# Performance work log

Hardware: AMD Instinct MI355X
Metric: run time of the kernel (lower is better)

## Reference

```python
import jax, jax.numpy as jnp
import numpy as np

N = 10000
IN_DIM = 1024
HID = 128
LAT = 64
E = 320000


def setup_inputs() -> dict:
    key = jax.random.key(0)
    ks = jax.random.split(key, 12)
    def glorot(k, shape):
        lim = float(np.sqrt(6.0 / (shape[0] + shape[1])))
        return jax.random.uniform(k, shape, jnp.float32, -lim, lim)
    x = jax.random.normal(ks[0], (N, IN_DIM), jnp.float32)
    edge_index = jax.random.randint(ks[1], (2, E), 0, N, jnp.int64)
    return {
        "x": x,
        "edge_index": edge_index,
        "W_enc1": glorot(ks[2], (IN_DIM, HID)), "b_enc1": jnp.zeros((HID,), jnp.float32),
        "W_enc2": glorot(ks[3], (HID, LAT)),   "b_enc2": jnp.zeros((LAT,), jnp.float32),
        "W_att1": glorot(ks[4], (LAT, HID)),   "b_att1": jnp.zeros((HID,), jnp.float32),
        "W_att2": glorot(ks[5], (HID, IN_DIM)),"b_att2": jnp.zeros((IN_DIM,), jnp.float32),
        "W_str":  glorot(ks[6], (LAT, LAT)),   "b_str":  jnp.zeros((LAT,), jnp.float32),
    }


def _gcn_norm(edge_index, n):
    # PyG GCNConv default: add self-loops, symmetric normalization
    loop = jnp.arange(n, dtype=edge_index.dtype)
    send = jnp.concatenate([edge_index[0], loop])
    recv = jnp.concatenate([edge_index[1], loop])
    deg = jax.ops.segment_sum(jnp.ones_like(recv, dtype=jnp.float32), recv, num_segments=n)
    dis = jnp.where(deg > 0, jax.lax.rsqrt(deg), 0.0)
    norm = dis[send] * dis[recv]  # [E+N]
    return send, recv, norm


def _gcn(x, W, b, send, recv, norm, n):
    h = x @ W                                  # [N, out]
    msg = h[send] * norm[:, None]              # gather + scale
    agg = jax.ops.segment_sum(msg, recv, num_segments=n)  # scatter-add
    return agg + b


def reference(x, edge_index, W_enc1, b_enc1, W_enc2, b_enc2,
              W_att1, b_att1, W_att2, b_att2, W_str, b_str):
    n = x.shape[0]
    send, recv, norm = _gcn_norm(edge_index, n)
    # encoder
    h = jax.nn.relu(_gcn(x, W_enc1, b_enc1, send, recv, norm, n))
    z = jax.nn.relu(_gcn(h, W_enc2, b_enc2, send, recv, norm, n))
    # attribute decoder
    a = jax.nn.relu(_gcn(z, W_att1, b_att1, send, recv, norm, n))
    attr_recon = jax.nn.relu(_gcn(a, W_att2, b_att2, send, recv, norm, n))
    # structure decoder
    s = jax.nn.relu(_gcn(z, W_str, b_str, send, recv, norm, n))
    struct_recon = s @ s.T  # [N, N]
    return (attr_recon, struct_recon, z)
```

## Files before the change

### kernel.cpp

```cpp
#include <hip/hip_runtime.h>
#include <hip/hip_bf16.h>

#define IN_DIM 1024
#define HID 128
#define LAT 64
#define DEGPAD 128

typedef __attribute__((ext_vector_type(8))) short bf16x8;
typedef __attribute__((ext_vector_type(4))) short bf16x4;
typedef __attribute__((ext_vector_type(4))) float f32x4;

#define W1T_OFF 0
#define W2T_OFF 131072
#define Wa1T_OFF 139264
#define Wa2T_OFF 147456
#define WsT_OFF 278528
#define WT_TOTAL 282624

__device__ __forceinline__ void splitf(float v, __hip_bfloat16& h, __hip_bfloat16& l) {
    h = __float2bfloat16(v);
    l = __float2bfloat16(v - __bfloat162float(h));
}


template<int AMODE, bool BIAS, bool RELU, bool DIS, bool SPLITOUT, bool NT>
__device__ void dev_gemm(float* smem, int bx, int byy,
        const __hip_bfloat16* __restrict__ Ahi, const __hip_bfloat16* __restrict__ Alo,
        const float* __restrict__ Af,
        const __hip_bfloat16* __restrict__ Bthi, const __hip_bfloat16* __restrict__ Btlo,
        const float* __restrict__ bias, const int* __restrict__ cursor,
        float* __restrict__ Cf, __hip_bfloat16* __restrict__ Chi, __hip_bfloat16* __restrict__ Clo,
        int M, int K, int ldc) {
    int tid = threadIdx.x;
    int w = tid >> 6, lane = tid & 63;
    int wr = w >> 1, wc = w & 1;
    int m0 = byy * 128, n0 = bx * 64;
    int lrow = lane & 15, lk = (lane >> 4) * 8;

    int arow[4];
    size_t aoff[4];
#pragma unroll
    for (int mi = 0; mi < 4; ++mi) {
        arow[mi] = m0 + wr * 64 + mi * 16 + lrow;
        aoff[mi] = (size_t)arow[mi] * K + lk;
    }
    size_t boff[2];
#pragma unroll
    for (int nj = 0; nj < 2; ++nj)
        boff[nj] = (size_t)(n0 + wc * 32 + nj * 16 + lrow) * K + lk;

    f32x4 acc[4][2] = {};

    for (int k0 = 0; k0 < K; k0 += 32) {
        bf16x8 bh[2], bl[2], ah[4], al[4];
#pragma unroll
        for (int nj = 0; nj < 2; ++nj) {
            bh[nj] = *(const bf16x8*)(Bthi + boff[nj] + k0);
            bl[nj] = *(const bf16x8*)(Btlo + boff[nj] + k0);
        }
        if constexpr (AMODE == 0) {
#pragma unroll
            for (int mi = 0; mi < 4; ++mi) {
                ah[mi] = *(const bf16x8*)(Ahi + aoff[mi] + k0);
                al[mi] = *(const bf16x8*)(Alo + aoff[mi] + k0);
            }
        } else {
#pragma unroll
            for (int mi = 0; mi < 4; ++mi) {
                float4 f0 = make_float4(0.f, 0.f, 0.f, 0.f), f1 = f0;
                if (arow[mi] < M) {
                    f0 = *(const float4*)(Af + aoff[mi] + k0);
                    f1 = *(const float4*)(Af + aoff[mi] + k0 + 4);
                }
                float ff[8] = {f0.x, f0.y, f0.z, f0.w, f1.x, f1.y, f1.z, f1.w};
                __attribute__((aligned(16))) __hip_bfloat16 hb[8], lb[8];
#pragma unroll
                for (int t = 0; t < 8; ++t) splitf(ff[t], hb[t], lb[t]);
                ah[mi] = *(const bf16x8*)hb;
                al[mi] = *(const bf16x8*)lb;
            }
        }
#pragma unroll
        for (int mi = 0; mi < 4; ++mi)
#pragma unroll
            for (int nj = 0; nj < 2; ++nj) {
                acc[mi][nj] = __builtin_amdgcn_mfma_f32_16x16x32_bf16(ah[mi], bh[nj], acc[mi][nj], 0, 0, 0);
                acc[mi][nj] = __builtin_amdgcn_mfma_f32_16x16x32_bf16(ah[mi], bl[nj], acc[mi][nj], 0, 0, 0);
                acc[mi][nj] = __builtin_amdgcn_mfma_f32_16x16x32_bf16(al[mi], bh[nj], acc[mi][nj], 0, 0, 0);
            }
    }

    int r0 = (lane >> 4) * 4;
#pragma unroll
    for (int mi = 0; mi < 4; ++mi)
#pragma unroll
        for (int nj = 0; nj < 2; ++nj) {
            int cl = wc * 32 + nj * 16 + lrow;
#pragma unroll
            for (int r = 0; r < 4; ++r) {
                int rl = wr * 64 + mi * 16 + r0 + r;
                smem[rl * 68 + cl] = acc[mi][nj][r];
            }
        }
    __syncthreads();

#pragma unroll
    for (int it = 0; it < 8; ++it) {
        int rl = it * 16 + (tid >> 4);
        int c4 = tid & 15;
        int row = m0 + rl;
        if (row < M) {
            int col = n0 + c4 * 4;
            float4 v = *(const float4*)&smem[rl * 68 + c4 * 4];
            if (BIAS) {
                float4 b = *(const float4*)&bias[col];
                v.x += b.x; v.y += b.y; v.z += b.z; v.w += b.w;
            }
            if (RELU) {
                v.x = fmaxf(v.x, 0.f); v.y = fmaxf(v.y, 0.f);
                v.z = fmaxf(v.z, 0.f); v.w = fmaxf(v.w, 0.f);
            }
            if (DIS) {
                float di = rsqrtf((float)(cursor[row] + 1));
                v.x *= di; v.y *= di; v.z *= di; v.w *= di;
            }
            if constexpr (SPLITOUT) {
                float vv[4] = {v.x, v.y, v.z, v.w};
                __attribute__((aligned(8))) __hip_bfloat16 hs[4], ls[4];
#pragma unroll
                for (int k = 0; k < 4; ++k) splitf(vv[k], hs[k], ls[k]);
                *(bf16x4*)&Chi[(size_t)row * ldc + col] = *(bf16x4*)hs;
                *(bf16x4*)&Clo[(size_t)row * ldc + col] = *(bf16x4*)ls;
            } else if constexpr (NT) {
                __builtin_nontemporal_store(*(const f32x4*)&v, (f32x4*)&Cf[(size_t)row * ldc + col]);
            } else {
                *(float4*)&Cf[(size_t)row * ldc + col] = v;
            }
        }
    }
    __syncthreads();
}


__device__ void dev_sst(float* smem, int bi, int bj,
                        const __hip_bfloat16* __restrict__ Shi, const __hip_bfloat16* __restrict__ Slo,
                        float* __restrict__ C, int M) {
    int tid = threadIdx.x;
    int w = tid >> 6, lane = tid & 63;
    int wr = w >> 1, wc = w & 1;
    int i0 = bi * 128 + wr * 64;
    int j0 = bj * 128 + wc * 64;
    int lrow = lane & 15, lk = (lane >> 4) * 8;

    f32x4 acc[4][4] = {};
#pragma unroll
    for (int ks = 0; ks < 2; ++ks) {
        bf16x8 ah[4], al[4], bh[4], bl[4];
#pragma unroll
        for (int mi = 0; mi < 4; ++mi) {
            size_t off = (size_t)(i0 + mi * 16 + lrow) * 64 + ks * 32 + lk;
            ah[mi] = *(const bf16x8*)(Shi + off);
            al[mi] = *(const bf16x8*)(Slo + off);
        }
#pragma unroll
        for (int nj = 0; nj < 4; ++nj) {
            size_t off = (size_t)(j0 + nj * 16 + lrow) * 64 + ks * 32 + lk;
            bh[nj] = *(const bf16x8*)(Shi + off);
            bl[nj] = *(const bf16x8*)(Slo + off);
        }
#pragma unroll
        for (int mi = 0; mi < 4; ++mi)
#pragma unroll
            for (int nj = 0; nj < 4; ++nj) {
                acc[mi][nj] = __builtin_amdgcn_mfma_f32_16x16x32_bf16(ah[mi], bh[nj], acc[mi][nj], 0, 0, 0);
                acc[mi][nj] = __builtin_amdgcn_mfma_f32_16x16x32_bf16(ah[mi], bl[nj], acc[mi][nj], 0, 0, 0);
                acc[mi][nj] = __builtin_amdgcn_mfma_f32_16x16x32_bf16(al[mi], bh[nj], acc[mi][nj], 0, 0, 0);
            }
    }

    int r0 = (lane >> 4) * 4;

    if (bi != bj) {
#pragma unroll
        for (int mi = 0; mi < 4; ++mi)
#pragma unroll
            for (int nj = 0; nj < 4; ++nj) {
                int orow = j0 + nj * 16 + lrow;
                int ocol = i0 + mi * 16 + r0;
                if (orow < M && ocol < M) {
                    f32x4 v = acc[mi][nj];
                    __builtin_nontemporal_store(v, (f32x4*)&C[(size_t)orow * M + ocol]);
                }
            }
    }

#pragma unroll
    for (int p = 0; p < 2; ++p) {
        if (wc == p) {
#pragma unroll
            for (int mi = 0; mi < 4; ++mi)
#pragma unroll
                for (int nj = 0; nj < 4; ++nj) {
                    int cl = nj * 16 + lrow;
#pragma unroll
                    for (int r = 0; r < 4; ++r) {
                        int rl = wr * 64 + mi * 16 + r0 + r;
                        smem[rl * 68 + cl] = acc[mi][nj][r];
                    }
                }
        }
        __syncthreads();
#pragma unroll
        for (int it = 0; it < 8; ++it) {
            int rl = it * 16 + (tid >> 4);
            int c4 = tid & 15;
            int row = bi * 128 + rl;
            int col = bj * 128 + p * 64 + c4 * 4;
            if (row < M && col < M) {
                float4 v = *(const float4*)&smem[rl * 68 + c4 * 4];
                __builtin_nontemporal_store(*(const f32x4*)&v, (f32x4*)&C[(size_t)row * M + col]);
            }
        }
        __syncthreads();
    }
}


__global__ __launch_bounds__(256) void k_prep(const float* __restrict__ W1, const float* __restrict__ W2,
                                              const float* __restrict__ Wa1, const float* __restrict__ Wa2,
                                              const float* __restrict__ Ws,
                                              __hip_bfloat16* __restrict__ hi, __hip_bfloat16* __restrict__ lo,
                                              const int* __restrict__ ei, int* cursor,
                                              int* __restrict__ colPad, int E) {
    int gtid = blockIdx.x * 256 + threadIdx.x;
    int gsz = gridDim.x * 256;
    for (int e = gtid; e < E; e += gsz) {
        int s = ei[e], r = ei[E + e];
        int slot = atomicAdd(&cursor[r], 1);
        if (slot < DEGPAD) colPad[(size_t)r * DEGPAD + slot] = s;
    }
    for (int idx = gtid; idx < WT_TOTAL; idx += gsz) {
        const float* src; int base, shK, Nc;
        if (idx < W2T_OFF)       { src = W1;  base = W1T_OFF;  shK = 10; Nc = 128; }
        else if (idx < Wa1T_OFF) { src = W2;  base = W2T_OFF;  shK = 7;  Nc = 64; }
        else if (idx < Wa2T_OFF) { src = Wa1; base = Wa1T_OFF; shK = 6;  Nc = 128; }
        else if (idx < WsT_OFF)  { src = Wa2; base = Wa2T_OFF; shK = 7;  Nc = 1024; }
        else                     { src = Ws;  base = WsT_OFF;  shK = 6;  Nc = 64; }
        int local = idx - base;
        int nn = local >> shK;
        int k = local & ((1 << shK) - 1);
        splitf(src[(size_t)k * Nc + nn], hi[idx], lo[idx]);
    }
}

__global__ __launch_bounds__(256) void k_g1(const float* __restrict__ x,
                                            const __hip_bfloat16* __restrict__ Whi,
                                            const __hip_bfloat16* __restrict__ Wlo,
                                            const int* __restrict__ cursor,
                                            float* __restrict__ t128, int M) {
    __shared__ float smem[128 * 68];
    int t = blockIdx.x;
    dev_gemm<1, false, false, true, false, false>(smem, t & 1, t >> 1,
        nullptr, nullptr, x, Whi + W1T_OFF, Wlo + W1T_OFF, nullptr, cursor,
        t128, nullptr, nullptr, M, 1024, 128);
}

template<int F, bool BIAS, bool RELU, int OMODE>
__global__ __launch_bounds__(256) void k_spmm(const float* __restrict__ Hin,
                                              const int* __restrict__ colPad,
                                              const int* __restrict__ cursor,
                                              const float* __restrict__ bias,
                                              float* __restrict__ out, float* __restrict__ out2,
                                              __hip_bfloat16* __restrict__ ohi,
                                              __hip_bfloat16* __restrict__ olo, int n) {
    constexpr int JW = F / 64;
    int i = (blockIdx.x * 256 + threadIdx.x) >> 6;
    int lane = threadIdx.x & 63;
    if (i >= n) return;
    int d = cursor[i];
    float di = rsqrtf((float)(d + 1));
    if (d > DEGPAD) d = DEGPAD;
    const int* cp = colPad + (size_t)i * DEGPAD;
    float acc[JW];
    const float* self = Hin + (size_t)i * F;
#pragma unroll
    for (int j = 0; j < JW; ++j) acc[j] = self[lane + 64 * j];

    int p = 0;
    for (; p + 8 <= d; p += 8) {
        int4 ca = *(const int4*)(cp + p);
        int4 cb = *(const int4*)(cp + p + 4);
        int cc[8] = {ca.x, ca.y, ca.z, ca.w, cb.x, cb.y, cb.z, cb.w};
        float vals[8][JW];
#pragma unroll
        for (int q = 0; q < 8; ++q) {
            const float* row = Hin + (size_t)cc[q] * F;
#pragma unroll
            for (int j = 0; j < JW; ++j) vals[q][j] = row[lane + 64 * j];
        }
#pragma unroll
        for (int q = 0; q < 8; ++q)
#pragma unroll
            for (int j = 0; j < JW; ++j) acc[j] += vals[q][j];
    }
    for (; p + 4 <= d; p += 4) {
        int4 ca = *(const int4*)(cp + p);
        int cc[4] = {ca.x, ca.y, ca.z, ca.w};
        float vals[4][JW];
#pragma unroll
        for (int q = 0; q < 4; ++q) {
            const float* row = Hin + (size_t)cc[q] * F;
#pragma unroll
            for (int j = 0; j < JW; ++j) vals[q][j] = row[lane + 64 * j];
        }
#pragma unroll
        for (int q = 0; q < 4; ++q)
#pragma unroll
            for (int j = 0; j < JW; ++j) acc[j] += vals[q][j];
    }
    for (; p < d; ++p) {
        const float* row = Hin + (size_t)cp[p] * F;
#pragma unroll
        for (int j = 0; j < JW; ++j) acc[j] += row[lane + 64 * j];
    }

#pragma unroll
    for (int j = 0; j < JW; ++j) {
        float r = acc[j] * di;
        if (BIAS) r += bias[lane + 64 * j];
        if (RELU) r = fmaxf(r, 0.f);
        size_t idx = (size_t)i * F + lane + 64 * j;
        if constexpr (OMODE == 1) {
            __hip_bfloat16 h, l;
            splitf(r, h, l);
            ohi[idx] = h; olo[idx] = l;
        } else {
            out[idx] = r;
            if constexpr (OMODE == 2) out2[idx] = r * di;
        }
    }
}

__global__ __launch_bounds__(256) void k_g2(const __hip_bfloat16* __restrict__ Hhi,
                                            const __hip_bfloat16* __restrict__ Hlo,
                                            const __hip_bfloat16* __restrict__ Whi,
                                            const __hip_bfloat16* __restrict__ Wlo,
                                            const int* __restrict__ cursor,
                                            float* __restrict__ t64, int M) {
    __shared__ float smem[128 * 68];
    dev_gemm<0, false, false, true, false, false>(smem, 0, blockIdx.x,
        Hhi, Hlo, nullptr, Whi + W2T_OFF, Wlo + W2T_OFF, nullptr, cursor,
        t64, nullptr, nullptr, M, 128, 64);
}

__global__ __launch_bounds__(256) void k_g34(const __hip_bfloat16* __restrict__ AZhi,
                                             const __hip_bfloat16* __restrict__ AZlo,
                                             const __hip_bfloat16* __restrict__ Whi,
                                             const __hip_bfloat16* __restrict__ Wlo,
                                             const float* __restrict__ ba1, const float* __restrict__ bs,
                                             const int* __restrict__ cursor,
                                             float* __restrict__ t128,
                                             __hip_bfloat16* __restrict__ Shi, __hip_bfloat16* __restrict__ Slo,
                                             int M, int Mpad) {
    __shared__ float smem[128 * 68];
    int nt2 = (Mpad / 128) * 2;
    int t = blockIdx.x;
    if (t < nt2)
        dev_gemm<0, true, true, true, false, false>(smem, t & 1, t >> 1,
            AZhi, AZlo, nullptr, Whi + Wa1T_OFF, Wlo + Wa1T_OFF, ba1, cursor,
            t128, nullptr, nullptr, M, 64, 128);
    else
        dev_gemm<0, true, true, false, true, false>(smem, 0, t - nt2,
            AZhi, AZlo, nullptr, Whi + WsT_OFF, Wlo + WsT_OFF, bs, nullptr,
            nullptr, Shi, Slo, M, 64, 64);
}

__global__ __launch_bounds__(256) void k_tail(const __hip_bfloat16* __restrict__ AAhi,
                                              const __hip_bfloat16* __restrict__ AAlo,
                                              const __hip_bfloat16* __restrict__ Whi,
                                              const __hip_bfloat16* __restrict__ Wlo,
                                              const float* __restrict__ ba2,
                                              const __hip_bfloat16* __restrict__ Shi,
                                              const __hip_bfloat16* __restrict__ Slo,
                                              float* __restrict__ attr, float* __restrict__ st,
                                              int M, int Mpad) {
    __shared__ float smem[128 * 68];
    int nt = Mpad / 128;
    int nG5 = 16 * nt;
    int t = blockIdx.x;
    if (t < nG5) {
        dev_gemm<0, true, true, false, false, true>(smem, t & 15, t >> 4,
            AAhi, AAlo, nullptr, Whi + Wa2T_OFF, Wlo + Wa2T_OFF, ba2, nullptr,
            attr, nullptr, nullptr, M, 128, 1024);
    } else {
        int tt = t - nG5;
        int bi = 0;
        while (tt >= nt - bi) { tt -= nt - bi; bi++; }
        dev_sst(smem, bi, bi + tt, Shi, Slo, st, M);
    }
}


extern "C" void kernel_launch(void* const* d_in, const int* in_sizes, int n_in,
                              void* d_out, int out_size, void* d_ws, size_t ws_size,
                              hipStream_t stream) {
    const float* x   = (const float*)d_in[0];
    const int*   ei  = (const int*)d_in[1];
    const float* W1  = (const float*)d_in[2];
    const float* b1  = (const float*)d_in[3];
    const float* W2  = (const float*)d_in[4];
    const float* b2  = (const float*)d_in[5];
    const float* Wa1 = (const float*)d_in[6];
    const float* ba1 = (const float*)d_in[7];
    const float* Wa2 = (const float*)d_in[8];
    const float* ba2 = (const float*)d_in[9];
    const float* Ws  = (const float*)d_in[10];
    const float* bs  = (const float*)d_in[11];

    int N = in_sizes[0] / IN_DIM;
    int E = in_sizes[1] / 2;
    int Mpad = ((N + 127) / 128) * 128;
    int nt = Mpad / 128;

    float* out  = (float*)d_out;
    float* attr = out;
    float* st   = out + (size_t)N * IN_DIM;
    float* zout = st + (size_t)N * N;

    char* basep = (char*)d_ws;
    size_t off = 0;
    auto alloc = [&](size_t bytes) -> void* {
        void* p = basep + off;
        off = (off + bytes + 255) & ~(size_t)255;
        return p;
    };
    int*   colPad = (int*)alloc((size_t)N * DEGPAD * 4);
    int*   cursor = (int*)alloc((size_t)N * 4);
    __hip_bfloat16* Whi = (__hip_bfloat16*)alloc((size_t)WT_TOTAL * 2);
    __hip_bfloat16* Wlo = (__hip_bfloat16*)alloc((size_t)WT_TOTAL * 2);
    float* t128 = (float*)alloc((size_t)N * 128 * 4);
    float* t64  = (float*)alloc((size_t)N * 64 * 4);
    float* zp   = (float*)alloc((size_t)N * 64 * 4);
    __hip_bfloat16* Hhi  = (__hip_bfloat16*)alloc((size_t)Mpad * 128 * 2);
    __hip_bfloat16* Hlo  = (__hip_bfloat16*)alloc((size_t)Mpad * 128 * 2);
    __hip_bfloat16* AZhi = (__hip_bfloat16*)alloc((size_t)Mpad * 64 * 2);
    __hip_bfloat16* AZlo = (__hip_bfloat16*)alloc((size_t)Mpad * 64 * 2);
    __hip_bfloat16* AAhi = (__hip_bfloat16*)alloc((size_t)Mpad * 128 * 2);
    __hip_bfloat16* AAlo = (__hip_bfloat16*)alloc((size_t)Mpad * 128 * 2);
    __hip_bfloat16* Shi  = (__hip_bfloat16*)alloc((size_t)Mpad * 64 * 2);
    __hip_bfloat16* Slo  = (__hip_bfloat16*)alloc((size_t)Mpad * 64 * 2);

    dim3 b256(256);
    int spmm_grid = (N * 64 + 255) / 256;

    hipMemsetAsync(cursor, 0, (size_t)N * 4, stream);
    k_prep<<<dim3(1280), b256, 0, stream>>>(W1, W2, Wa1, Wa2, Ws, Whi, Wlo, ei, cursor, colPad, E);
    k_g1<<<dim3(2 * nt), b256, 0, stream>>>(x, Whi, Wlo, cursor, t128, N);
    k_spmm<128, true, true, 1><<<dim3(spmm_grid), b256, 0, stream>>>(
        t128, colPad, cursor, b1, nullptr, nullptr, Hhi, Hlo, N);
    k_g2<<<dim3(nt), b256, 0, stream>>>(Hhi, Hlo, Whi, Wlo, cursor, t64, N);
    k_spmm<64, true, true, 2><<<dim3(spmm_grid), b256, 0, stream>>>(
        t64, colPad, cursor, b2, zout, zp, nullptr, nullptr, N);
    k_spmm<64, false, false, 1><<<dim3(spmm_grid), b256, 0, stream>>>(
        zp, colPad, cursor, nullptr, nullptr, nullptr, AZhi, AZlo, N);
    k_g34<<<dim3(3 * nt), b256, 0, stream>>>(AZhi, AZlo, Whi, Wlo, ba1, bs, cursor, t128, Shi, Slo, N, Mpad);
    k_spmm<128, false, false, 1><<<dim3(spmm_grid), b256, 0, stream>>>(
        t128, colPad, cursor, nullptr, nullptr, nullptr, AAhi, AAlo, N);
    k_tail<<<dim3(16 * nt + nt * (nt + 1) / 2), b256, 0, stream>>>(
        AAhi, AAlo, Whi, Wlo, ba2, Shi, Slo, attr, st, N, Mpad);
}
```

Baseline: 299.7 us.

## Overlap final SpMM with part of S·Sᵀ tiles and vectorize 128-wide SpMM

Merges the last 128-wide aggregation with a share of the structure-decoder S·Sᵀ tiles into one launch, so the independent GEMM tiles fill the GPU while the gather-bound SpMM runs. The remaining SST tiles, capped at 640, run alongside the attribute-decoder GEMM in the tail kernel. The 128-feature SpMM now loads float2 per lane and writes packed bf16 pairs, and the 64-feature path becomes its own kernel. The split point is fixed, so load balance between the two launches depends on problem size, and the merged kernel carries the GEMM's shared-memory footprint into its SpMM blocks, which may lower their occupancy.

```diff
diff --git a/kernel.cpp b/kernel.cpp
--- a/kernel.cpp
+++ b/kernel.cpp
@@ -226,6 +226,134 @@
 }
 
 
+template<bool BIAS, bool RELU, int OMODE>
+__device__ __forceinline__ void dev_spmm128(int i, int lane,
+        const float* __restrict__ Hin, const int* __restrict__ colPad,
+        const int* __restrict__ cursor, const float* __restrict__ bias,
+        float* __restrict__ out,
+        __hip_bfloat16* __restrict__ ohi, __hip_bfloat16* __restrict__ olo, int n) {
+    if (i >= n) return;
+    int d = cursor[i];
+    float di = rsqrtf((float)(d + 1));
+    if (d > DEGPAD) d = DEGPAD;
+    const int* cp = colPad + (size_t)i * DEGPAD;
+    float2 acc = ((const float2*)(Hin + (size_t)i * 128))[lane];
+
+    int p = 0;
+    for (; p + 8 <= d; p += 8) {
+        int4 ca = *(const int4*)(cp + p);
+        int4 cb = *(const int4*)(cp + p + 4);
+        int cc[8] = {ca.x, ca.y, ca.z, ca.w, cb.x, cb.y, cb.z, cb.w};
+        float2 v[8];
+#pragma unroll
+        for (int q = 0; q < 8; ++q)
+            v[q] = ((const float2*)(Hin + (size_t)cc[q] * 128))[lane];
+#pragma unroll
+        for (int q = 0; q < 8; ++q) { acc.x += v[q].x; acc.y += v[q].y; }
+    }
+    for (; p + 4 <= d; p += 4) {
+        int4 ca = *(const int4*)(cp + p);
+        int cc[4] = {ca.x, ca.y, ca.z, ca.w};
+        float2 v[4];
+#pragma unroll
+        for (int q = 0; q < 4; ++q)
+            v[q] = ((const float2*)(Hin + (size_t)cc[q] * 128))[lane];
+#pragma unroll
+        for (int q = 0; q < 4; ++q) { acc.x += v[q].x; acc.y += v[q].y; }
+    }
+    for (; p < d; ++p) {
+        float2 v = ((const float2*)(Hin + (size_t)cp[p] * 128))[lane];
+        acc.x += v.x; acc.y += v.y;
+    }
+
+    float rx = acc.x * di, ry = acc.y * di;
+    if (BIAS) {
+        float2 b = ((const float2*)bias)[lane];
+        rx += b.x; ry += b.y;
+    }
+    if (RELU) { rx = fmaxf(rx, 0.f); ry = fmaxf(ry, 0.f); }
+    size_t base = (size_t)i * 128 + 2 * lane;
+    if constexpr (OMODE == 1) {
+        __hip_bfloat16 h0, l0, h1, l1;
+        splitf(rx, h0, l0);
+        splitf(ry, h1, l1);
+        union { __hip_bfloat16 b[2]; unsigned u; } uh, ul;
+        uh.b[0] = h0; uh.b[1] = h1;
+        ul.b[0] = l0; ul.b[1] = l1;
+        *(unsigned*)&ohi[base] = uh.u;
+        *(unsigned*)&olo[base] = ul.u;
+    } else {
+        *(float2*)&out[base] = make_float2(rx, ry);
+    }
+}
+
+template<bool BIAS, bool RELU, int OMODE>
+__global__ __launch_bounds__(256) void k_spmm128(const float* __restrict__ Hin,
+                                                 const int* __restrict__ colPad,
+                                                 const int* __restrict__ cursor,
+                                                 const float* __restrict__ bias,
+                                                 float* __restrict__ out,
+                                                 __hip_bfloat16* __restrict__ ohi,
+                                                 __hip_bfloat16* __restrict__ olo, int n) {
+    int i = (blockIdx.x * 256 + threadIdx.x) >> 6;
+    dev_spmm128<BIAS, RELU, OMODE>(i, threadIdx.x & 63, Hin, colPad, cursor, bias, out, ohi, olo, n);
+}
+
+
+template<bool BIAS, bool RELU, int OMODE>
+__global__ __launch_bounds__(256) void k_spmm64(const float* __restrict__ Hin,
+                                                const int* __restrict__ colPad,
+                                                const int* __restrict__ cursor,
+                                                const float* __restrict__ bias,
+                                                float* __restrict__ out, float* __restrict__ out2,
+                                                __hip_bfloat16* __restrict__ ohi,
+                                                __hip_bfloat16* __restrict__ olo, int n) {
+    int i = (blockIdx.x * 256 + threadIdx.x) >> 6;
+    int lane = threadIdx.x & 63;
+    if (i >= n) return;
+    int d = cursor[i];
+    float di = rsqrtf((float)(d + 1));
+    if (d > DEGPAD) d = DEGPAD;
+    const int* cp = colPad + (size_t)i * DEGPAD;
+    float acc = Hin[(size_t)i * 64 + lane];
+
+    int p = 0;
+    for (; p + 8 <= d; p += 8) {
+        int4 ca = *(const int4*)(cp + p);
+        int4 cb = *(const int4*)(cp + p + 4);
+        int cc[8] = {ca.x, ca.y, ca.z, ca.w, cb.x, cb.y, cb.z, cb.w};
+        float v[8];
+#pragma unroll
+        for (int q = 0; q < 8; ++q) v[q] = Hin[(size_t)cc[q] * 64 + lane];
+#pragma unroll
+        for (int q = 0; q < 8; ++q) acc += v[q];
+    }
+    for (; p + 4 <= d; p += 4) {
+        int4 ca = *(const int4*)(cp + p);
+        int cc[4] = {ca.x, ca.y, ca.z, ca.w};
+        float v[4];
+#pragma unroll
+        for (int q = 0; q < 4; ++q) v[q] = Hin[(size_t)cc[q] * 64 + lane];
+#pragma unroll
+        for (int q = 0; q < 4; ++q) acc += v[q];
+    }
+    for (; p < d; ++p) acc += Hin[(size_t)cp[p] * 64 + lane];
+
+    float r = acc * di;
+    if (BIAS) r += bias[lane];
+    if (RELU) r = fmaxf(r, 0.f);
+    size_t idx = (size_t)i * 64 + lane;
+    if constexpr (OMODE == 1) {
+        __hip_bfloat16 h, l;
+        splitf(r, h, l);
+        ohi[idx] = h; olo[idx] = l;
+    } else {
+        out[idx] = r;
+        if constexpr (OMODE == 2) out2[idx] = r * di;
+    }
+}
+
+
 __global__ __launch_bounds__(256) void k_prep(const float* __restrict__ W1, const float* __restrict__ W2,
                                               const float* __restrict__ Wa1, const float* __restrict__ Wa2,
                                               const float* __restrict__ Ws,
@@ -263,82 +391,6 @@
     dev_gemm<1, false, false, true, false, false>(smem, t & 1, t >> 1,
         nullptr, nullptr, x, Whi + W1T_OFF, Wlo + W1T_OFF, nullptr, cursor,
         t128, nullptr, nullptr, M, 1024, 128);
-}
-
-template<int F, bool BIAS, bool RELU, int OMODE>
-__global__ __launch_bounds__(256) void k_spmm(const float* __restrict__ Hin,
-                                              const int* __restrict__ colPad,
-                                              const int* __restrict__ cursor,
-                                              const float* __restrict__ bias,
-                                              float* __restrict__ out, float* __restrict__ out2,
-                                              __hip_bfloat16* __restrict__ ohi,
-                                              __hip_bfloat16* __restrict__ olo, int n) {
-    constexpr int JW = F / 64;
-    int i = (blockIdx.x * 256 + threadIdx.x) >> 6;
-    int lane = threadIdx.x & 63;
-    if (i >= n) return;
-    int d = cursor[i];
-    float di = rsqrtf((float)(d + 1));
-    if (d > DEGPAD) d = DEGPAD;
-    const int* cp = colPad + (size_t)i * DEGPAD;
-    float acc[JW];
-    const float* self = Hin + (size_t)i * F;
-#pragma unroll
-    for (int j = 0; j < JW; ++j) acc[j] = self[lane + 64 * j];
-
-    int p = 0;
-    for (; p + 8 <= d; p += 8) {
-        int4 ca = *(const int4*)(cp + p);
-        int4 cb = *(const int4*)(cp + p + 4);
-        int cc[8] = {ca.x, ca.y, ca.z, ca.w, cb.x, cb.y, cb.z, cb.w};
-        float vals[8][JW];
-#pragma unroll
-        for (int q = 0; q < 8; ++q) {
-            const float* row = Hin + (size_t)cc[q] * F;
-#pragma unroll
-            for (int j = 0; j < JW; ++j) vals[q][j] = row[lane + 64 * j];
-        }
-#pragma unroll
-        for (int q = 0; q < 8; ++q)
-#pragma unroll
-            for (int j = 0; j < JW; ++j) acc[j] += vals[q][j];
-    }
-    for (; p + 4 <= d; p += 4) {
-        int4 ca = *(const int4*)(cp + p);
-        int cc[4] = {ca.x, ca.y, ca.z, ca.w};
-        float vals[4][JW];
-#pragma unroll
-        for (int q = 0; q < 4; ++q) {
-            const float* row = Hin + (size_t)cc[q] * F;
-#pragma unroll
-            for (int j = 0; j < JW; ++j) vals[q][j] = row[lane + 64 * j];
-        }
-#pragma unroll
-        for (int q = 0; q < 4; ++q)
-#pragma unroll
-            for (int j = 0; j < JW; ++j) acc[j] += vals[q][j];
-    }
-    for (; p < d; ++p) {
-        const float* row = Hin + (size_t)cp[p] * F;
-#pragma unroll
-        for (int j = 0; j < JW; ++j) acc[j] += row[lane + 64 * j];
-    }
-
-#pragma unroll
-    for (int j = 0; j < JW; ++j) {
-        float r = acc[j] * di;
-        if (BIAS) r += bias[lane + 64 * j];
-        if (RELU) r = fmaxf(r, 0.f);
-        size_t idx = (size_t)i * F + lane + 64 * j;
-        if constexpr (OMODE == 1) {
-            __hip_bfloat16 h, l;
-            splitf(r, h, l);
-            ohi[idx] = h; olo[idx] = l;
-        } else {
-            out[idx] = r;
-            if constexpr (OMODE == 2) out2[idx] = r * di;
-        }
-    }
 }
 
 __global__ __launch_bounds__(256) void k_g2(const __hip_bfloat16* __restrict__ Hhi,
@@ -375,15 +427,39 @@
             nullptr, Shi, Slo, M, 64, 64);
 }
 
-__global__ __launch_bounds__(256) void k_tail(const __hip_bfloat16* __restrict__ AAhi,
-                                              const __hip_bfloat16* __restrict__ AAlo,
-                                              const __hip_bfloat16* __restrict__ Whi,
-                                              const __hip_bfloat16* __restrict__ Wlo,
-                                              const float* __restrict__ ba2,
-                                              const __hip_bfloat16* __restrict__ Shi,
-                                              const __hip_bfloat16* __restrict__ Slo,
-                                              float* __restrict__ attr, float* __restrict__ st,
-                                              int M, int Mpad) {
+__global__ __launch_bounds__(256) void k_sp4sst(const float* __restrict__ t128,
+                                                const int* __restrict__ colPad,
+                                                const int* __restrict__ cursor,
+                                                __hip_bfloat16* __restrict__ AAhi,
+                                                __hip_bfloat16* __restrict__ AAlo,
+                                                const __hip_bfloat16* __restrict__ Shi,
+                                                const __hip_bfloat16* __restrict__ Slo,
+                                                float* __restrict__ st,
+                                                int M, int Mpad, int nsp, int sstN) {
+    __shared__ float smem[128 * 68];
+    int t = blockIdx.x;
+    if (t < nsp) {
+        int i = (t * 256 + threadIdx.x) >> 6;
+        dev_spmm128<false, false, 1>(i, threadIdx.x & 63, t128, colPad, cursor,
+                                     nullptr, nullptr, AAhi, AAlo, M);
+    } else {
+        int s = t - nsp;
+        int nt = Mpad / 128;
+        int bi = 0;
+        while (s >= nt - bi) { s -= nt - bi; bi++; }
+        dev_sst(smem, bi, bi + s, Shi, Slo, st, M);
+    }
+}
+
+__global__ __launch_bounds__(256) void k_g5sst(const __hip_bfloat16* __restrict__ AAhi,
+                                               const __hip_bfloat16* __restrict__ AAlo,
+                                               const __hip_bfloat16* __restrict__ Whi,
+                                               const __hip_bfloat16* __restrict__ Wlo,
+                                               const float* __restrict__ ba2,
+                                               const __hip_bfloat16* __restrict__ Shi,
+                                               const __hip_bfloat16* __restrict__ Slo,
+                                               float* __restrict__ attr, float* __restrict__ st,
+                                               int M, int Mpad, int sstBase) {
     __shared__ float smem[128 * 68];
     int nt = Mpad / 128;
     int nG5 = 16 * nt;
@@ -393,10 +469,10 @@
             AAhi, AAlo, nullptr, Whi + Wa2T_OFF, Wlo + Wa2T_OFF, ba2, nullptr,
             attr, nullptr, nullptr, M, 128, 1024);
     } else {
-        int tt = t - nG5;
+        int s = sstBase + (t - nG5);
         int bi = 0;
-        while (tt >= nt - bi) { tt -= nt - bi; bi++; }
-        dev_sst(smem, bi, bi + tt, Shi, Slo, st, M);
+        while (s >= nt - bi) { s -= nt - bi; bi++; }
+        dev_sst(smem, bi, bi + s, Shi, Slo, st, M);
     }
 }
 
@@ -421,6 +497,9 @@
     int E = in_sizes[1] / 2;
     int Mpad = ((N + 127) / 128) * 128;
     int nt = Mpad / 128;
+    int Tri = nt * (nt + 1) / 2;
+    int sstC = Tri < 640 ? Tri : 640;
+    int sstB = Tri - sstC;
 
     float* out  = (float*)d_out;
     float* attr = out;
@@ -456,16 +535,16 @@
     hipMemsetAsync(cursor, 0, (size_t)N * 4, stream);
     k_prep<<<dim3(1280), b256, 0, stream>>>(W1, W2, Wa1, Wa2, Ws, Whi, Wlo, ei, cursor, colPad, E);
     k_g1<<<dim3(2 * nt), b256, 0, stream>>>(x, Whi, Wlo, cursor, t128, N);
-    k_spmm<128, true, true, 1><<<dim3(spmm_grid), b256, 0, stream>>>(
-        t128, colPad, cursor, b1, nullptr, nullptr, Hhi, Hlo, N);
+    k_spmm128<true, true, 1><<<dim3(spmm_grid), b256, 0, stream>>>(
+        t128, colPad, cursor, b1, nullptr, Hhi, Hlo, N);
     k_g2<<<dim3(nt), b256, 0, stream>>>(Hhi, Hlo, Whi, Wlo, cursor, t64, N);
-    k_spmm<64, true, true, 2><<<dim3(spmm_grid), b256, 0, stream>>>(
+    k_spmm64<true, true, 2><<<dim3(spmm_grid), b256, 0, stream>>>(
         t64, colPad, cursor, b2, zout, zp, nullptr, nullptr, N);
-    k_spmm<64, false, false, 1><<<dim3(spmm_grid), b256, 0, stream>>>(
+    k_spmm64<false, false, 1><<<dim3(spmm_grid), b256, 0, stream>>>(
         zp, colPad, cursor, nullptr, nullptr, nullptr, AZhi, AZlo, N);
     k_g34<<<dim3(3 * nt), b256, 0, stream>>>(AZhi, AZlo, Whi, Wlo, ba1, bs, cursor, t128, Shi, Slo, N, Mpad);
-    k_spmm<128, false, false, 1><<<dim3(spmm_grid), b256, 0, stream>>>(
-        t128, colPad, cursor, nullptr, nullptr, nullptr, AAhi, AAlo, N);
-    k_tail<<<dim3(16 * nt + nt * (nt + 1) / 2), b256, 0, stream>>>(
-        AAhi, AAlo, Whi, Wlo, ba2, Shi, Slo, attr, st, N, Mpad);
-}
+    k_sp4sst<<<dim3(spmm_grid + sstB), b256, 0, stream>>>(
+        t128, colPad, cursor, AAhi, AAlo, Shi, Slo, st, N, Mpad, spmm_grid, sstB);
+    k_g5sst<<<dim3(16 * nt + sstC), b256, 0, stream>>>(
+        AAhi, AAlo, Whi, Wlo, ba2, Shi, Slo, attr, st, N, Mpad, sstB);
+}
```

Result: slower. 374.8 us (+25.1%).
